# Performance work log

Hardware: AMD Instinct MI355X
Metric: run time of the kernel (lower is better)

Reference implementation:

```python
import jax, jax.numpy as jnp
import numpy as np

N = 50000      # nodes
E = 800000     # directed edges (before self loops)
B = 64         # graphs in batch
F_IN = 128     # input_dim
POS = 16       # pos_dim
H = 4          # heads
C = 64         # hidden_dim (per head)
HC = H * C     # 256
OUT = 128      # output_dim
ENH = F_IN + POS
EPS = 1e-5
NEG_SLOPE = 0.2


def setup_inputs() -> dict:
    key = jax.random.key(0)
    ks = jax.random.split(key, 20)
    s = 0.05
    inp = {
        "x": jax.random.normal(ks[0], (N, F_IN), jnp.float32),
        "edge_index": jax.random.randint(ks[1], (2, E), 0, N, jnp.int32),
        "batch": (jnp.arange(N, dtype=jnp.int32) // ((N + B - 1) // B)).astype(jnp.int32),
        "W_pos": jax.random.normal(ks[2], (2, POS), jnp.float32) * s,
        "b_pos": jnp.zeros((POS,), jnp.float32),
        "W1": jax.random.normal(ks[3], (ENH, HC), jnp.float32) * s,
        "a_src1": jax.random.normal(ks[4], (H, C), jnp.float32) * s,
        "a_dst1": jax.random.normal(ks[5], (H, C), jnp.float32) * s,
        "b1": jnp.zeros((HC,), jnp.float32),
        "gamma1": jnp.ones((HC,), jnp.float32),
        "beta1": jnp.zeros((HC,), jnp.float32),
        "W2": jax.random.normal(ks[6], (HC, HC), jnp.float32) * s,
        "a_src2": jax.random.normal(ks[7], (H, C), jnp.float32) * s,
        "a_dst2": jax.random.normal(ks[8], (H, C), jnp.float32) * s,
        "b2": jnp.zeros((HC,), jnp.float32),
        "gamma2": jnp.ones((HC,), jnp.float32),
        "beta2": jnp.zeros((HC,), jnp.float32),
        "W_fc": jax.random.normal(ks[9], (HC, OUT), jnp.float32) * s,
        "b_fc": jnp.zeros((OUT,), jnp.float32),
    }
    return inp


def _positions(batch):
    # vectorized equivalent of _generate_positions (grid layout per graph)
    ones = jnp.ones((N,), jnp.float32)
    counts = jax.ops.segment_sum(ones, batch, num_segments=B)          # [B]
    starts = jnp.cumsum(counts) - counts                               # [B]
    i = jnp.arange(N, dtype=jnp.float32) - starts[batch]               # index within graph
    gs = jnp.ceil(jnp.sqrt(counts)).astype(jnp.int32)                  # grid size per graph
    g = gs[batch]
    ii = i.astype(jnp.int32)
    row = ii // g
    col = ii % g
    denom = jnp.maximum(g - 1, 1).astype(jnp.float32)
    return jnp.stack([row.astype(jnp.float32) / denom,
                      col.astype(jnp.float32) / denom], axis=1)        # [N, 2]


def _gat(x, W, a_src, a_dst, bias, src, dst):
    # PyG GATConv (concat heads, add_self_loops already in src/dst)
    h = (x @ W).reshape(N, H, C)                                       # [N,H,C]
    alpha_s = jnp.sum(h * a_src, axis=-1)                              # [N,H]
    alpha_d = jnp.sum(h * a_dst, axis=-1)                              # [N,H]
    e = jax.nn.leaky_relu(alpha_s[src] + alpha_d[dst], NEG_SLOPE)      # [Etot,H]
    e_max = jax.ops.segment_max(e, dst, num_segments=N)                # [N,H]
    e_max = jax.lax.stop_gradient(jnp.where(jnp.isfinite(e_max), e_max, 0.0))
    ex = jnp.exp(e - e_max[dst])
    denom = jax.ops.segment_sum(ex, dst, num_segments=N)               # [N,H]
    alpha = ex / denom[dst]                                            # softmax over incoming edges
    msg = h[src] * alpha[:, :, None]                                   # [Etot,H,C]
    out = jax.ops.segment_sum(msg, dst, num_segments=N)                # [N,H,C]
    return out.reshape(N, HC) + bias


def _bn(x, gamma, beta):
    m = jnp.mean(x, axis=0)
    v = jnp.var(x, axis=0)
    return gamma * (x - m) * jax.lax.rsqrt(v + EPS) + beta


def reference(x, edge_index, batch, W_pos, b_pos,
              W1, a_src1, a_dst1, b1, gamma1, beta1,
              W2, a_src2, a_dst2, b2, gamma2, beta2,
              W_fc, b_fc):
    pos = _positions(batch)
    pe = pos @ W_pos + b_pos                                           # [N,POS]
    h = jnp.concatenate([x, pe], axis=1)                               # [N,ENH]
    loops = jnp.arange(N, dtype=edge_index.dtype)
    src = jnp.concatenate([edge_index[0], loops])
    dst = jnp.concatenate([edge_index[1], loops])
    h = jax.nn.elu(_bn(_gat(h, W1, a_src1, a_dst1, b1, src, dst), gamma1, beta1))
    h = jax.nn.elu(_bn(_gat(h, W2, a_src2, a_dst2, b2, src, dst), gamma2, beta2))
    # global mean pool per graph
    counts = jax.ops.segment_sum(jnp.ones((N,), h.dtype), batch, num_segments=B)
    pooled = jax.ops.segment_sum(h, batch, num_segments=B) / counts[:, None]
    return pooled @ W_fc + b_fc                                        # [B,OUT]
```

## Files before the change

kernel.cpp:

```cpp
#include <hip/hip_runtime.h>
#include <math.h>

#define ENH_PAD 160
#define POSD 16
#define DEG_CAP 64
#define NSLICE 8
#define KNODES 8

typedef __attribute__((ext_vector_type(8))) __bf16 bf16x8;
typedef __attribute__((ext_vector_type(4))) float f32x4;

__device__ __forceinline__ unsigned short f2bf(float f){
  unsigned int u = __float_as_uint(f);
  u += 0x7FFF + ((u >> 16) & 1);
  return (unsigned short)(u >> 16);
}
__device__ __forceinline__ float bf2f(unsigned short u){
  return __uint_as_float(((unsigned int)u) << 16);
}

__global__ void k_front(const int* __restrict__ batch, int* __restrict__ starts,
                        const int* __restrict__ src, const int* __restrict__ dst,
                        int* __restrict__ cnt, int* __restrict__ csr_src,
                        float* __restrict__ bnP, float* __restrict__ pooled,
                        int N, int E){
  int i = blockIdx.x * blockDim.x + threadIdx.x;
  if (i < 2 * NSLICE * 512) bnP[i] = 0.f;
  if (i < 64 * 256) pooled[i] = 0.f;
  if (i < N){
    int bi = batch[i];
    int bp = (i == 0) ? -1 : batch[i - 1];
    for (int b = bp + 1; b <= bi; ++b) starts[b] = i;
    if (i == N - 1){
      for (int b = bi + 1; b <= 64; ++b) starts[b] = N;
    }
  }
  if (i < E){
    int d = dst[i];
    int slot = atomicAdd(&cnt[d], 1);
    csr_src[(size_t)d * DEG_CAP + slot] = src[i];
  }
}

__global__ __launch_bounds__(256) void k_prep(
    const float* __restrict__ x, const int* __restrict__ batch,
    const int* __restrict__ starts,
    const float* __restrict__ W_pos, const float* __restrict__ b_pos,
    unsigned short* __restrict__ h0,
    const float* __restrict__ W1, const float* __restrict__ W2,
    unsigned short* __restrict__ W1t, unsigned short* __restrict__ W2t,
    int N, int nb4){
  if ((int)blockIdx.x < nb4){
    int n = blockIdx.x * 4 + (threadIdx.x >> 6);
    if (n >= N) return;
    int t = threadIdx.x & 63;
    unsigned short* hrow = h0 + (size_t)n * ENH_PAD;
    if (t < 32){
      const float4* xs = (const float4*)(x + (size_t)n * 128);
      float4 v = xs[t];
      ushort4 o; o.x = f2bf(v.x); o.y = f2bf(v.y); o.z = f2bf(v.z); o.w = f2bf(v.w);
      ((ushort4*)hrow)[t] = o;
    } else if (t < 48){
      int k = t - 32;
      int b = batch[n];
      int st = starts[b];
      int c = starts[b + 1] - st;
      int g = (int)ceilf(sqrtf((float)c));
      int dd = g - 1; if (dd < 1) dd = 1;
      float idn = 1.0f / (float)dd;
      int i = n - st;
      int row = i / g;
      int col = i - row * g;
      float pe = (float)row * idn * W_pos[k] + (float)col * idn * W_pos[POSD + k] + b_pos[k];
      hrow[128 + k] = f2bf(pe);
    } else {
      hrow[144 + (t - 48)] = 0;
    }
  } else {
    int idx = (blockIdx.x - nb4) * 256 + threadIdx.x;
    const int n1 = 256 * ENH_PAD;
    if (idx < n1){
      int n = idx / ENH_PAD, k = idx - n * ENH_PAD;
      W1t[idx] = f2bf((k < 144) ? W1[(size_t)k * 256 + n] : 0.f);
    } else {
      int j = idx - n1;
      if (j < 256 * 256){
        int n = j >> 8, k = j & 255;
        W2t[j] = f2bf(W2[(size_t)k * 256 + n]);
      }
    }
  }
}

#define LDST 40
__global__ __launch_bounds__(256) void k_mfma_gemm(
    const unsigned short* __restrict__ A, const unsigned short* __restrict__ Bt,
    unsigned short* __restrict__ C,
    const float* __restrict__ a_src, const float* __restrict__ a_dst,
    float* __restrict__ alpS, float* __restrict__ alpD, int M, int Kp){
  __shared__ unsigned short As[128 * LDST];
  __shared__ unsigned short Bs[128 * LDST];
  int t = threadIdx.x;
  int lane = t & 63, wave = t >> 6;
  int wm = (wave >> 1) * 64, wn = (wave & 1) * 64;
  int quad = lane >> 4, l16 = lane & 15;
  int row0 = blockIdx.x * 128;
  int n0 = blockIdx.y * 128;

  f32x4 acc[4][4] = {};

  int eA0 = t, eA1 = t + 256;
  for (int kk = 0; kk < Kp; kk += 32){
    #pragma unroll
    for (int rep = 0; rep < 2; ++rep){
      int e = rep ? eA1 : eA0;
      int r = e >> 2, s = e & 3;
      int grow = row0 + r;
      uint4 va = make_uint4(0, 0, 0, 0);
      if (grow < M) va = *(const uint4*)(A + (size_t)grow * Kp + kk + s * 8);
      *(uint4*)&As[r * LDST + s * 8] = va;
      uint4 vb = *(const uint4*)(Bt + (size_t)(n0 + r) * Kp + kk + s * 8);
      *(uint4*)&Bs[r * LDST + s * 8] = vb;
    }
    __syncthreads();
    bf16x8 af[4], bfr[4];
    #pragma unroll
    for (int i = 0; i < 4; ++i)
      af[i] = *(const bf16x8*)&As[(wm + i * 16 + l16) * LDST + quad * 8];
    #pragma unroll
    for (int j = 0; j < 4; ++j)
      bfr[j] = *(const bf16x8*)&Bs[(wn + j * 16 + l16) * LDST + quad * 8];
    #pragma unroll
    for (int i = 0; i < 4; ++i)
      #pragma unroll
      for (int j = 0; j < 4; ++j)
        acc[i][j] = __builtin_amdgcn_mfma_f32_16x16x32_bf16(af[i], bfr[j], acc[i][j], 0, 0, 0);
    __syncthreads();
  }
  #pragma unroll
  for (int i = 0; i < 4; ++i){
    int rbase = row0 + wm + i * 16 + quad * 4;
    #pragma unroll
    for (int j = 0; j < 4; ++j){
      int col = n0 + wn + j * 16 + l16;
      #pragma unroll
      for (int r = 0; r < 4; ++r){
        int row = rbase + r;
        if (row < M) C[(size_t)row * 256 + col] = f2bf(acc[i][j][r]);
      }
    }
  }
  int hda = (n0 + wn) >> 6;
  float asw[4], adw[4];
  #pragma unroll
  for (int j = 0; j < 4; ++j){
    int c = n0 + wn + j * 16 + l16;
    asw[j] = a_src[c];
    adw[j] = a_dst[c];
  }
  #pragma unroll
  for (int i = 0; i < 4; ++i){
    #pragma unroll
    for (int r = 0; r < 4; ++r){
      int row = row0 + wm + i * 16 + quad * 4 + r;
      float ps = acc[i][0][r] * asw[0] + acc[i][1][r] * asw[1]
               + acc[i][2][r] * asw[2] + acc[i][3][r] * asw[3];
      float pd = acc[i][0][r] * adw[0] + acc[i][1][r] * adw[1]
               + acc[i][2][r] * adw[2] + acc[i][3][r] * adw[3];
      ps += __shfl_xor(ps, 1); ps += __shfl_xor(ps, 2);
      ps += __shfl_xor(ps, 4); ps += __shfl_xor(ps, 8);
      pd += __shfl_xor(pd, 1); pd += __shfl_xor(pd, 2);
      pd += __shfl_xor(pd, 4); pd += __shfl_xor(pd, 8);
      if (l16 == 0 && row < M){
        alpS[row * 4 + hda] = ps;
        alpD[row * 4 + hda] = pd;
      }
    }
  }
}

__global__ __launch_bounds__(256) void k_aggregate(const unsigned short* __restrict__ hlin,
                                                   const float* __restrict__ alpS,
                                                   const float* __restrict__ alpD,
                                                   const int* __restrict__ cnt,
                                                   const int* __restrict__ csr_src,
                                                   const float* __restrict__ bias,
                                                   unsigned short* __restrict__ outb,
                                                   float* __restrict__ bnP, int N){
  __shared__ float rs[4][256];
  __shared__ float rq[4][256];
  int wv = threadIdx.x >> 6;
  int lane = threadIdx.x & 63;
  int hd = lane >> 4;
  int hd2 = lane & 3;
  int eloc = lane >> 2;
  const unsigned short* hbase = hlin + (size_t)lane * 4;
  float4 bv = *(const float4*)(bias + lane * 4);

  float s0 = 0.f, s1 = 0.f, s2 = 0.f, s3 = 0.f;
  float q0 = 0.f, q1 = 0.f, q2 = 0.f, q3 = 0.f;

  int nbase = (blockIdx.x * 4 + wv) * KNODES;
  for (int k = 0; k < KNODES; ++k){
    int n = nbase + k;
    if (n >= N) break;
    int beg = n << 6;
    int deg = cnt[n];
    int total = deg + 1;
    float ad2 = alpD[n * 4 + hd2];
    float lsum = 0.f;
    float a0 = 0.f, a1 = 0.f, a2 = 0.f, a3 = 0.f;

    int full = total & ~15;
    for (int base = 0; base < full; base += 16){
      int e = base + eloc;
      int s = (e < deg) ? csr_src[beg + e] : n;
      float xv = alpS[s * 4 + hd2] + ad2;
      float sc = (xv >= 0.f) ? xv : 0.2f * xv;
      float p = __expf(sc);
      lsum += p;
      uint2 v[16];
      #pragma unroll
      for (int j2 = 0; j2 < 16; ++j2){
        int sj = __shfl(s, j2 << 2);
        v[j2] = *(const uint2*)(hbase + (size_t)sj * 256);
      }
      #pragma unroll
      for (int j2 = 0; j2 < 16; ++j2){
        float pj = __shfl(p, (j2 << 2) | hd);
        a0 += pj * __uint_as_float(v[j2].x << 16);
        a1 += pj * __uint_as_float(v[j2].x & 0xFFFF0000u);
        a2 += pj * __uint_as_float(v[j2].y << 16);
        a3 += pj * __uint_as_float(v[j2].y & 0xFFFF0000u);
      }
    }
    int rem = total - full;
    if (rem){
      int e = full + eloc;
      int s = n;
      float p = 0.f;
      if (eloc < rem){
        if (e < deg) s = csr_src[beg + e];
        float xv = alpS[s * 4 + hd2] + ad2;
        float sc = (xv >= 0.f) ? xv : 0.2f * xv;
        p = __expf(sc);
      }
      lsum += p;
      #pragma unroll
      for (int g = 0; g < 4; ++g){
        if (g * 4 < rem){
          uint2 v[4];
          #pragma unroll
          for (int q = 0; q < 4; ++q){
            int j2 = g * 4 + q;
            int sj = __shfl(s, j2 << 2);
            v[q] = *(const uint2*)(hbase + (size_t)sj * 256);
          }
          #pragma unroll
          for (int q = 0; q < 4; ++q){
            int j2 = g * 4 + q;
            float pj = __shfl(p, (j2 << 2) | hd);
            a0 += pj * __uint_as_float(v[q].x << 16);
            a1 += pj * __uint_as_float(v[q].x & 0xFFFF0000u);
            a2 += pj * __uint_as_float(v[q].y << 16);
            a3 += pj * __uint_as_float(v[q].y & 0xFFFF0000u);
          }
        }
      }
    }
    lsum += __shfl_xor(lsum, 4);
    lsum += __shfl_xor(lsum, 8);
    lsum += __shfl_xor(lsum, 16);
    lsum += __shfl_xor(lsum, 32);
    float lh = __shfl(lsum, hd);
    float inv = 1.0f / lh;
    ushort4 o;
    o.x = f2bf(a0 * inv + bv.x);
    o.y = f2bf(a1 * inv + bv.y);
    o.z = f2bf(a2 * inv + bv.z);
    o.w = f2bf(a3 * inv + bv.w);
    *(ushort4*)(outb + (size_t)n * 256 + lane * 4) = o;
    float f0 = bf2f(o.x), f1 = bf2f(o.y), f2 = bf2f(o.z), f3 = bf2f(o.w);
    s0 += f0; s1 += f1; s2 += f2; s3 += f3;
    q0 += f0 * f0; q1 += f1 * f1; q2 += f2 * f2; q3 += f3 * f3;
  }

  int c0 = lane * 4;
  rs[wv][c0 + 0] = s0; rs[wv][c0 + 1] = s1;
  rs[wv][c0 + 2] = s2; rs[wv][c0 + 3] = s3;
  rq[wv][c0 + 0] = q0; rq[wv][c0 + 1] = q1;
  rq[wv][c0 + 2] = q2; rq[wv][c0 + 3] = q3;
  __syncthreads();
  int t = threadIdx.x;
  float s = rs[0][t] + rs[1][t] + rs[2][t] + rs[3][t];
  float q = rq[0][t] + rq[1][t] + rq[2][t] + rq[3][t];
  float* bp = bnP + (size_t)(blockIdx.x & (NSLICE - 1)) * 512;
  atomicAdd(&bp[t], s);
  atomicAdd(&bp[256 + t], q);
}

__global__ __launch_bounds__(256) void k_bn_elu_bf16(
    const unsigned short* __restrict__ in, const float* __restrict__ bnP,
    const float* __restrict__ gamma, const float* __restrict__ beta,
    unsigned short* __restrict__ outb, int N, float invN){
  __shared__ float scs[256], shs[256];
  int t = threadIdx.x;
  float s = 0.f, q = 0.f;
  #pragma unroll
  for (int j = 0; j < NSLICE; ++j){
    s += bnP[j * 512 + t];
    q += bnP[j * 512 + 256 + t];
  }
  float mean = s * invN;
  float var = q * invN - mean * mean;
  float inv = rsqrtf(var + 1e-5f);
  float g = gamma[t];
  scs[t] = g * inv;
  shs[t] = beta[t] - mean * g * inv;
  __syncthreads();
  int idx8 = blockIdx.x * blockDim.x + t;
  int total8 = N * 32;
  for (; idx8 < total8; idx8 += gridDim.x * blockDim.x){
    int c0 = (idx8 * 8) & 255;
    uint4 raw = *(const uint4*)(in + (size_t)idx8 * 8);
    unsigned int rw[4] = {raw.x, raw.y, raw.z, raw.w};
    uint4 outw;
    unsigned int* ow = (unsigned int*)&outw;
    #pragma unroll
    for (int h = 0; h < 4; ++h){
      unsigned int res = 0;
      #pragma unroll
      for (int k = 0; k < 2; ++k){
        int c = c0 + h * 2 + k;
        unsigned short bits = (unsigned short)((rw[h] >> (16 * k)) & 0xFFFF);
        float y = scs[c] * bf2f(bits) + shs[c];
        y = (y > 0.f) ? y : (__expf(y) - 1.f);
        res |= ((unsigned int)f2bf(y)) << (16 * k);
      }
      ow[h] = res;
    }
    *(uint4*)(outb + (size_t)idx8 * 8) = outw;
  }
}

__global__ __launch_bounds__(256) void k_bn_elu_pool(
    const unsigned short* __restrict__ in, const float* __restrict__ bnP,
    const float* __restrict__ gamma, const float* __restrict__ beta,
    const int* __restrict__ batch,
    float* __restrict__ pooled, int N, float invN){
  int t = threadIdx.x;
  float s = 0.f, q = 0.f;
  #pragma unroll
  for (int j = 0; j < NSLICE; ++j){
    s += bnP[j * 512 + t];
    q += bnP[j * 512 + 256 + t];
  }
  float mean = s * invN;
  float var = q * invN - mean * mean;
  float inv = rsqrtf(var + 1e-5f);
  float g = gamma[t];
  float scl = g * inv;
  float shf = beta[t] - mean * scl;
  int nb = gridDim.x;
  int rows = (N + nb - 1) / nb;
  int r0 = blockIdx.x * rows, r1 = min(r0 + rows, N);
  float acc = 0.f; int cur = -1;
  for (int r = r0; r < r1; ++r){
    float y = scl * bf2f(in[(size_t)r * 256 + t]) + shf;
    y = (y > 0.f) ? y : (__expf(y) - 1.f);
    int b = batch[r];
    if (b != cur){
      if (cur >= 0) atomicAdd(&pooled[cur * 256 + t], acc);
      acc = 0.f; cur = b;
    }
    acc += y;
  }
  if (cur >= 0) atomicAdd(&pooled[cur * 256 + t], acc);
}

__global__ __launch_bounds__(128) void k_final(const float* __restrict__ pooled,
                                               const int* __restrict__ starts,
                                               const float* __restrict__ W_fc,
                                               const float* __restrict__ b_fc,
                                               float* __restrict__ out){
  __shared__ float pm[256];
  int b = blockIdx.x;
  int t = threadIdx.x;
  int c = starts[b + 1] - starts[b];
  float ic = (c > 0) ? 1.0f / (float)c : 0.f;
  pm[t] = pooled[b * 256 + t] * ic;
  pm[t + 128] = pooled[b * 256 + t + 128] * ic;
  __syncthreads();
  float acc = b_fc[t];
  #pragma unroll 4
  for (int cc = 0; cc < 256; ++cc) acc += pm[cc] * W_fc[cc * 128 + t];
  out[b * 128 + t] = acc;
}

extern "C" void kernel_launch(void* const* d_in, const int* in_sizes, int n_in,
                              void* d_out, int out_size, void* d_ws, size_t ws_size,
                              hipStream_t stream){
  const float* x      = (const float*)d_in[0];
  const int*   eidx   = (const int*)  d_in[1];
  const int*   batch  = (const int*)  d_in[2];
  const float* W_pos  = (const float*)d_in[3];
  const float* b_pos  = (const float*)d_in[4];
  const float* W1     = (const float*)d_in[5];
  const float* a_src1 = (const float*)d_in[6];
  const float* a_dst1 = (const float*)d_in[7];
  const float* b1     = (const float*)d_in[8];
  const float* gamma1 = (const float*)d_in[9];
  const float* beta1  = (const float*)d_in[10];
  const float* W2     = (const float*)d_in[11];
  const float* a_src2 = (const float*)d_in[12];
  const float* a_dst2 = (const float*)d_in[13];
  const float* b2     = (const float*)d_in[14];
  const float* gamma2 = (const float*)d_in[15];
  const float* beta2  = (const float*)d_in[16];
  const float* W_fc   = (const float*)d_in[17];
  const float* b_fc   = (const float*)d_in[18];
  float* out = (float*)d_out;

  const int N = in_sizes[0] / 128;
  const int E = in_sizes[1] / 2;
  const int* esrc = eidx;
  const int* edst = eidx + E;

  char* w = (char*)d_ws;
  size_t off = 0;
  auto alloc = [&](size_t bytes) -> void* {
    void* p = w + off;
    off = (off + bytes + 255) & ~(size_t)255;
    return p;
  };
  unsigned short* h0   = (unsigned short*)alloc((size_t)N * 256 * 2);
  unsigned short* X2b  = h0;
  unsigned short* X1b  = (unsigned short*)alloc((size_t)N * 256 * 2);
  unsigned short* A1b  = (unsigned short*)alloc((size_t)N * 256 * 2);
  float* alpS    = (float*)alloc((size_t)N * 4 * 4);
  float* alpD    = (float*)alloc((size_t)N * 4 * 4);
  int*   starts  = (int*)  alloc(65 * 4);
  int*   cnt     = (int*)  alloc((size_t)N * 4);
  int*   csr_src = (int*)  alloc((size_t)N * DEG_CAP * 4);
  float* bnP     = (float*)alloc((size_t)2 * NSLICE * 512 * 4);
  float* pooled  = (float*)alloc(64 * 256 * 4);
  unsigned short* W1t = (unsigned short*)alloc(256 * ENH_PAD * 2);
  unsigned short* W2t = (unsigned short*)alloc(256 * 256 * 2);
  float* bnP1 = bnP, *bnP2 = bnP + NSLICE * 512;

  hipMemsetAsync(cnt, 0, (size_t)N * 4, stream);

  int nb4 = (N + 3) / 4;
  int nbagg = (N + KNODES * 4 - 1) / (KNODES * 4);
  const int packb = (256 * ENH_PAD + 256 * 256 + 255) / 256;

  k_front<<<(E + 255) / 256, 256, 0, stream>>>(batch, starts, esrc, edst, cnt, csr_src,
                                               bnP, pooled, N, E);
  k_prep<<<nb4 + packb, 256, 0, stream>>>(x, batch, starts, W_pos, b_pos, h0,
                                          W1, W2, W1t, W2t, N, nb4);

  dim3 ggrid((N + 127) / 128, 2);
  const float invN = 1.0f / (float)N;

  k_mfma_gemm<<<ggrid, 256, 0, stream>>>(h0, W1t, X1b, a_src1, a_dst1, alpS, alpD, N, ENH_PAD);
  k_aggregate<<<nbagg, 256, 0, stream>>>(X1b, alpS, alpD, cnt, csr_src, b1, A1b, bnP1, N);
  k_bn_elu_bf16<<<512, 256, 0, stream>>>(A1b, bnP1, gamma1, beta1, X2b, N, invN);

  k_mfma_gemm<<<ggrid, 256, 0, stream>>>(X2b, W2t, X1b, a_src2, a_dst2, alpS, alpD, N, 256);
  k_aggregate<<<nbagg, 256, 0, stream>>>(X1b, alpS, alpD, cnt, csr_src, b2, A1b, bnP2, N);
  k_bn_elu_pool<<<512, 256, 0, stream>>>(A1b, bnP2, gamma2, beta2, batch, pooled, N, invN);

  k_final<<<64, 128, 0, stream>>>(pooled, starts, W_fc, b_fc, out);
}
```

Baseline: 428.1 us.

## Fuse CSR build and node prep into one init kernel; retune aggregate granularity

Merges the edge-bucketing front kernel and the feature-prep kernel into a single launch. The per-graph starts array it depended on is replaced by binary searches over the sorted batch array, done in prep and in the final kernel. This removes one launch and the dependency between the two. Separately, KNODES drops from 8 to 2 so the aggregate kernel has more blocks with fewer nodes each, and NSLICE doubles the BN partial-sum slices. The cost is a redundant binary search per node thread and more partial-sum slices to reduce.

```diff
diff --git a/kernel.cpp b/kernel.cpp
--- a/kernel.cpp
+++ b/kernel.cpp
@@ -4,8 +4,8 @@
 #define ENH_PAD 160
 #define POSD 16
 #define DEG_CAP 64
-#define NSLICE 8
-#define KNODES 8
+#define NSLICE 16
+#define KNODES 2
 
 typedef __attribute__((ext_vector_type(8))) __bf16 bf16x8;
 typedef __attribute__((ext_vector_type(4))) float f32x4;
@@ -18,40 +18,38 @@
 __device__ __forceinline__ float bf2f(unsigned short u){
   return __uint_as_float(((unsigned int)u) << 16);
 }
-
-__global__ void k_front(const int* __restrict__ batch, int* __restrict__ starts,
-                        const int* __restrict__ src, const int* __restrict__ dst,
-                        int* __restrict__ cnt, int* __restrict__ csr_src,
-                        float* __restrict__ bnP, float* __restrict__ pooled,
-                        int N, int E){
-  int i = blockIdx.x * blockDim.x + threadIdx.x;
-  if (i < 2 * NSLICE * 512) bnP[i] = 0.f;
-  if (i < 64 * 256) pooled[i] = 0.f;
-  if (i < N){
-    int bi = batch[i];
-    int bp = (i == 0) ? -1 : batch[i - 1];
-    for (int b = bp + 1; b <= bi; ++b) starts[b] = i;
-    if (i == N - 1){
-      for (int b = bi + 1; b <= 64; ++b) starts[b] = N;
-    }
-  }
-  if (i < E){
-    int d = dst[i];
-    int slot = atomicAdd(&cnt[d], 1);
-    csr_src[(size_t)d * DEG_CAP + slot] = src[i];
-  }
-}
-
-__global__ __launch_bounds__(256) void k_prep(
-    const float* __restrict__ x, const int* __restrict__ batch,
-    const int* __restrict__ starts,
+__device__ __forceinline__ int lbound(const int* __restrict__ batch, int N, int b){
+  int lo = 0, hi = N;
+  while (lo < hi){
+    int mid = (lo + hi) >> 1;
+    if (batch[mid] < b) lo = mid + 1; else hi = mid;
+  }
+  return lo;
+}
+
+__global__ __launch_bounds__(256) void k_init(
+    const int* __restrict__ batch,
+    const int* __restrict__ src, const int* __restrict__ dst,
+    int* __restrict__ cnt, int* __restrict__ csr_src,
+    float* __restrict__ bnP, float* __restrict__ pooled,
+    const float* __restrict__ x,
     const float* __restrict__ W_pos, const float* __restrict__ b_pos,
     unsigned short* __restrict__ h0,
     const float* __restrict__ W1, const float* __restrict__ W2,
     unsigned short* __restrict__ W1t, unsigned short* __restrict__ W2t,
-    int N, int nb4){
-  if ((int)blockIdx.x < nb4){
-    int n = blockIdx.x * 4 + (threadIdx.x >> 6);
+    int N, int E, int nfb, int nb4){
+  int bx = blockIdx.x;
+  if (bx < nfb){
+    int i = bx * 256 + threadIdx.x;
+    if (i < 2 * NSLICE * 512) bnP[i] = 0.f;
+    if (i < 64 * 256) pooled[i] = 0.f;
+    if (i < E){
+      int d = dst[i];
+      int slot = atomicAdd(&cnt[d], 1);
+      csr_src[(size_t)d * DEG_CAP + slot] = src[i];
+    }
+  } else if (bx < nfb + nb4){
+    int n = (bx - nfb) * 4 + (threadIdx.x >> 6);
     if (n >= N) return;
     int t = threadIdx.x & 63;
     unsigned short* hrow = h0 + (size_t)n * ENH_PAD;
@@ -63,8 +61,8 @@
     } else if (t < 48){
       int k = t - 32;
       int b = batch[n];
-      int st = starts[b];
-      int c = starts[b + 1] - st;
+      int st = lbound(batch, N, b);
+      int c  = lbound(batch, N, b + 1) - st;
       int g = (int)ceilf(sqrtf((float)c));
       int dd = g - 1; if (dd < 1) dd = 1;
       float idn = 1.0f / (float)dd;
@@ -77,7 +75,7 @@
       hrow[144 + (t - 48)] = 0;
     }
   } else {
-    int idx = (blockIdx.x - nb4) * 256 + threadIdx.x;
+    int idx = (bx - nfb - nb4) * 256 + threadIdx.x;
     const int n1 = 256 * ENH_PAD;
     if (idx < n1){
       int n = idx / ENH_PAD, k = idx - n * ENH_PAD;
@@ -201,6 +199,7 @@
   float q0 = 0.f, q1 = 0.f, q2 = 0.f, q3 = 0.f;
 
   int nbase = (blockIdx.x * 4 + wv) * KNODES;
+  #pragma unroll
   for (int k = 0; k < KNODES; ++k){
     int n = nbase + k;
     if (n >= N) break;
@@ -379,14 +378,14 @@
 }
 
 __global__ __launch_bounds__(128) void k_final(const float* __restrict__ pooled,
-                                               const int* __restrict__ starts,
+                                               const int* __restrict__ batch,
                                                const float* __restrict__ W_fc,
                                                const float* __restrict__ b_fc,
-                                               float* __restrict__ out){
+                                               float* __restrict__ out, int N){
   __shared__ float pm[256];
   int b = blockIdx.x;
   int t = threadIdx.x;
-  int c = starts[b + 1] - starts[b];
+  int c = lbound(batch, N, b + 1) - lbound(batch, N, b);
   float ic = (c > 0) ? 1.0f / (float)c : 0.f;
   pm[t] = pooled[b * 256 + t] * ic;
   pm[t + 128] = pooled[b * 256 + t + 128] * ic;
@@ -439,7 +438,6 @@
   unsigned short* A1b  = (unsigned short*)alloc((size_t)N * 256 * 2);
   float* alpS    = (float*)alloc((size_t)N * 4 * 4);
   float* alpD    = (float*)alloc((size_t)N * 4 * 4);
-  int*   starts  = (int*)  alloc(65 * 4);
   int*   cnt     = (int*)  alloc((size_t)N * 4);
   int*   csr_src = (int*)  alloc((size_t)N * DEG_CAP * 4);
   float* bnP     = (float*)alloc((size_t)2 * NSLICE * 512 * 4);
@@ -450,14 +448,14 @@
 
   hipMemsetAsync(cnt, 0, (size_t)N * 4, stream);
 
-  int nb4 = (N + 3) / 4;
-  int nbagg = (N + KNODES * 4 - 1) / (KNODES * 4);
+  const int nfb = (E + 255) / 256;
+  const int nb4 = (N + 3) / 4;
   const int packb = (256 * ENH_PAD + 256 * 256 + 255) / 256;
-
-  k_front<<<(E + 255) / 256, 256, 0, stream>>>(batch, starts, esrc, edst, cnt, csr_src,
-                                               bnP, pooled, N, E);
-  k_prep<<<nb4 + packb, 256, 0, stream>>>(x, batch, starts, W_pos, b_pos, h0,
-                                          W1, W2, W1t, W2t, N, nb4);
+  const int nbagg = (N + KNODES * 4 - 1) / (KNODES * 4);
+
+  k_init<<<nfb + nb4 + packb, 256, 0, stream>>>(batch, esrc, edst, cnt, csr_src,
+                                                bnP, pooled, x, W_pos, b_pos, h0,
+                                                W1, W2, W1t, W2t, N, E, nfb, nb4);
 
   dim3 ggrid((N + 127) / 128, 2);
   const float invN = 1.0f / (float)N;
@@ -470,5 +468,5 @@
   k_aggregate<<<nbagg, 256, 0, stream>>>(X1b, alpS, alpD, cnt, csr_src, b2, A1b, bnP2, N);
   k_bn_elu_pool<<<512, 256, 0, stream>>>(A1b, bnP2, gamma2, beta2, batch, pooled, N, invN);
 
-  k_final<<<64, 128, 0, stream>>>(pooled, starts, W_fc, b_fc, out);
-}
+  k_final<<<64, 128, 0, stream>>>(pooled, batch, W_fc, b_fc, out, N);
+}
```

Result: slower. 455.9 us (+6.5%).

## Fold positional encoding into GEMM epilogue and merge init kernels

Applied to the files above, without the earlier changes.

Precomputes the product of the positional projection with the matching rows of W1 as three 256-vectors. The first GEMM then runs with K=128 on bf16 x only and adds row/col-scaled terms in its epilogue, which removes the padded 160-wide h0 build. The front and prep kernels are merged into one launch. Aggregation now uses fewer nodes per wave (more blocks), BN partial slices double, and the layer-2 input gets a separate buffer. The epilogue recomputes grid positions per row, which adds some integer and sqrt work per tile.

```diff
diff --git a/kernel.cpp b/kernel.cpp
--- a/kernel.cpp
+++ b/kernel.cpp
@@ -1,11 +1,10 @@
 #include <hip/hip_runtime.h>
 #include <math.h>
 
-#define ENH_PAD 160
 #define POSD 16
 #define DEG_CAP 64
-#define NSLICE 8
-#define KNODES 8
+#define NSLICE 16
+#define KNODES 2
 
 typedef __attribute__((ext_vector_type(8))) __bf16 bf16x8;
 typedef __attribute__((ext_vector_type(4))) float f32x4;
@@ -19,85 +18,77 @@
   return __uint_as_float(((unsigned int)u) << 16);
 }
 
-__global__ void k_front(const int* __restrict__ batch, int* __restrict__ starts,
-                        const int* __restrict__ src, const int* __restrict__ dst,
-                        int* __restrict__ cnt, int* __restrict__ csr_src,
-                        float* __restrict__ bnP, float* __restrict__ pooled,
-                        int N, int E){
-  int i = blockIdx.x * blockDim.x + threadIdx.x;
-  if (i < 2 * NSLICE * 512) bnP[i] = 0.f;
-  if (i < 64 * 256) pooled[i] = 0.f;
-  if (i < N){
-    int bi = batch[i];
-    int bp = (i == 0) ? -1 : batch[i - 1];
-    for (int b = bp + 1; b <= bi; ++b) starts[b] = i;
-    if (i == N - 1){
-      for (int b = bi + 1; b <= 64; ++b) starts[b] = N;
-    }
-  }
-  if (i < E){
-    int d = dst[i];
-    int slot = atomicAdd(&cnt[d], 1);
-    csr_src[(size_t)d * DEG_CAP + slot] = src[i];
-  }
-}
-
-__global__ __launch_bounds__(256) void k_prep(
-    const float* __restrict__ x, const int* __restrict__ batch,
-    const int* __restrict__ starts,
+__global__ __launch_bounds__(256) void k_init(
+    const int* __restrict__ batch, int* __restrict__ starts,
+    const int* __restrict__ src, const int* __restrict__ dst,
+    int* __restrict__ cnt, int* __restrict__ csr_src,
+    float* __restrict__ bnP, float* __restrict__ pooled,
+    const float* __restrict__ x, unsigned short* __restrict__ xb,
     const float* __restrict__ W_pos, const float* __restrict__ b_pos,
-    unsigned short* __restrict__ h0,
     const float* __restrict__ W1, const float* __restrict__ W2,
     unsigned short* __restrict__ W1t, unsigned short* __restrict__ W2t,
-    int N, int nb4){
-  if ((int)blockIdx.x < nb4){
-    int n = blockIdx.x * 4 + (threadIdx.x >> 6);
-    if (n >= N) return;
-    int t = threadIdx.x & 63;
-    unsigned short* hrow = h0 + (size_t)n * ENH_PAD;
-    if (t < 32){
-      const float4* xs = (const float4*)(x + (size_t)n * 128);
-      float4 v = xs[t];
-      ushort4 o; o.x = f2bf(v.x); o.y = f2bf(v.y); o.z = f2bf(v.z); o.w = f2bf(v.w);
-      ((ushort4*)hrow)[t] = o;
-    } else if (t < 48){
-      int k = t - 32;
-      int b = batch[n];
-      int st = starts[b];
-      int c = starts[b + 1] - st;
-      int g = (int)ceilf(sqrtf((float)c));
-      int dd = g - 1; if (dd < 1) dd = 1;
-      float idn = 1.0f / (float)dd;
-      int i = n - st;
-      int row = i / g;
-      int col = i - row * g;
-      float pe = (float)row * idn * W_pos[k] + (float)col * idn * W_pos[POSD + k] + b_pos[k];
-      hrow[128 + k] = f2bf(pe);
-    } else {
-      hrow[144 + (t - 48)] = 0;
-    }
+    float* __restrict__ uvw,
+    int N, int E, int nfb, int nxb){
+  int bx = blockIdx.x;
+  int t = threadIdx.x;
+  if (bx < nfb){
+    int i = bx * 256 + t;
+    if (i < 2 * NSLICE * 512) bnP[i] = 0.f;
+    if (i < 64 * 256) pooled[i] = 0.f;
+    if (i < N){
+      int bi = batch[i];
+      int bp = (i == 0) ? -1 : batch[i - 1];
+      for (int b = bp + 1; b <= bi; ++b) starts[b] = i;
+      if (i == N - 1){
+        for (int b = bi + 1; b <= 64; ++b) starts[b] = N;
+      }
+    }
+    if (i < E){
+      int d = dst[i];
+      int slot = atomicAdd(&cnt[d], 1);
+      csr_src[(size_t)d * DEG_CAP + slot] = src[i];
+    }
+  } else if (bx < nfb + nxb){
+    size_t idx8 = (size_t)(bx - nfb) * 256 + t;
+    if (idx8 * 8 < (size_t)N * 128){
+      const float4* xs = (const float4*)(x + idx8 * 8);
+      float4 v0 = xs[0], v1 = xs[1];
+      ushort4 o0, o1;
+      o0.x = f2bf(v0.x); o0.y = f2bf(v0.y); o0.z = f2bf(v0.z); o0.w = f2bf(v0.w);
+      o1.x = f2bf(v1.x); o1.y = f2bf(v1.y); o1.z = f2bf(v1.z); o1.w = f2bf(v1.w);
+      ushort4* od = (ushort4*)(xb + idx8 * 8);
+      od[0] = o0; od[1] = o1;
+    }
+  } else if (bx < nfb + nxb + 128){
+    int idx = (bx - nfb - nxb) * 256 + t;
+    int n = idx >> 7, k = idx & 127;
+    W1t[idx] = f2bf(W1[(size_t)k * 256 + n]);
+  } else if (bx < nfb + nxb + 128 + 256){
+    int j = (bx - nfb - nxb - 128) * 256 + t;
+    int n = j >> 8, k = j & 255;
+    W2t[j] = f2bf(W2[(size_t)k * 256 + n]);
   } else {
-    int idx = (blockIdx.x - nb4) * 256 + threadIdx.x;
-    const int n1 = 256 * ENH_PAD;
-    if (idx < n1){
-      int n = idx / ENH_PAD, k = idx - n * ENH_PAD;
-      W1t[idx] = f2bf((k < 144) ? W1[(size_t)k * 256 + n] : 0.f);
-    } else {
-      int j = idx - n1;
-      if (j < 256 * 256){
-        int n = j >> 8, k = j & 255;
-        W2t[j] = f2bf(W2[(size_t)k * 256 + n]);
-      }
-    }
+    float u = 0.f, v = 0.f, wv = 0.f;
+    #pragma unroll
+    for (int k = 0; k < POSD; ++k){
+      float wc = W1[(size_t)(128 + k) * 256 + t];
+      u  += W_pos[k] * wc;
+      v  += W_pos[POSD + k] * wc;
+      wv += b_pos[k] * wc;
+    }
+    uvw[t] = u; uvw[256 + t] = v; uvw[512 + t] = wv;
   }
 }
 
 #define LDST 40
+template<int POSC>
 __global__ __launch_bounds__(256) void k_mfma_gemm(
     const unsigned short* __restrict__ A, const unsigned short* __restrict__ Bt,
     unsigned short* __restrict__ C,
     const float* __restrict__ a_src, const float* __restrict__ a_dst,
-    float* __restrict__ alpS, float* __restrict__ alpD, int M, int Kp){
+    float* __restrict__ alpS, float* __restrict__ alpD, int M, int Kp,
+    const float* __restrict__ uvw, const int* __restrict__ batch,
+    const int* __restrict__ starts){
   __shared__ unsigned short As[128 * LDST];
   __shared__ unsigned short Bs[128 * LDST];
   int t = threadIdx.x;
@@ -137,6 +128,38 @@
         acc[i][j] = __builtin_amdgcn_mfma_f32_16x16x32_bf16(af[i], bfr[j], acc[i][j], 0, 0, 0);
     __syncthreads();
   }
+
+  if (POSC){
+    float uu[4], vv[4], ww[4];
+    #pragma unroll
+    for (int j = 0; j < 4; ++j){
+      int col = n0 + wn + j * 16 + l16;
+      uu[j] = uvw[col]; vv[j] = uvw[256 + col]; ww[j] = uvw[512 + col];
+    }
+    #pragma unroll
+    for (int i = 0; i < 4; ++i){
+      #pragma unroll
+      for (int r = 0; r < 4; ++r){
+        int row = row0 + wm + i * 16 + quad * 4 + r;
+        if (row < M){
+          int b = batch[row];
+          int st = starts[b];
+          int cc = starts[b + 1] - st;
+          int g = (int)ceilf(sqrtf((float)cc));
+          int dd = g - 1; if (dd < 1) dd = 1;
+          float idn = 1.0f / (float)dd;
+          int ii = row - st;
+          int irow = ii / g;
+          int icol = ii - irow * g;
+          float rn = (float)irow * idn, cn = (float)icol * idn;
+          #pragma unroll
+          for (int j = 0; j < 4; ++j)
+            acc[i][j][r] += rn * uu[j] + cn * vv[j] + ww[j];
+        }
+      }
+    }
+  }
+
   #pragma unroll
   for (int i = 0; i < 4; ++i){
     int rbase = row0 + wm + i * 16 + quad * 4;
@@ -201,6 +224,7 @@
   float q0 = 0.f, q1 = 0.f, q2 = 0.f, q3 = 0.f;
 
   int nbase = (blockIdx.x * 4 + wv) * KNODES;
+  #pragma unroll
   for (int k = 0; k < KNODES; ++k){
     int n = nbase + k;
     if (n >= N) break;
@@ -433,10 +457,10 @@
     off = (off + bytes + 255) & ~(size_t)255;
     return p;
   };
-  unsigned short* h0   = (unsigned short*)alloc((size_t)N * 256 * 2);
-  unsigned short* X2b  = h0;
+  unsigned short* xb   = (unsigned short*)alloc((size_t)N * 128 * 2);
   unsigned short* X1b  = (unsigned short*)alloc((size_t)N * 256 * 2);
   unsigned short* A1b  = (unsigned short*)alloc((size_t)N * 256 * 2);
+  unsigned short* X2b  = (unsigned short*)alloc((size_t)N * 256 * 2);
   float* alpS    = (float*)alloc((size_t)N * 4 * 4);
   float* alpD    = (float*)alloc((size_t)N * 4 * 4);
   int*   starts  = (int*)  alloc(65 * 4);
@@ -444,29 +468,31 @@
   int*   csr_src = (int*)  alloc((size_t)N * DEG_CAP * 4);
   float* bnP     = (float*)alloc((size_t)2 * NSLICE * 512 * 4);
   float* pooled  = (float*)alloc(64 * 256 * 4);
-  unsigned short* W1t = (unsigned short*)alloc(256 * ENH_PAD * 2);
+  unsigned short* W1t = (unsigned short*)alloc(256 * 128 * 2);
   unsigned short* W2t = (unsigned short*)alloc(256 * 256 * 2);
+  float* uvw = (float*)alloc(3 * 256 * 4);
   float* bnP1 = bnP, *bnP2 = bnP + NSLICE * 512;
 
   hipMemsetAsync(cnt, 0, (size_t)N * 4, stream);
 
-  int nb4 = (N + 3) / 4;
-  int nbagg = (N + KNODES * 4 - 1) / (KNODES * 4);
-  const int packb = (256 * ENH_PAD + 256 * 256 + 255) / 256;
-
-  k_front<<<(E + 255) / 256, 256, 0, stream>>>(batch, starts, esrc, edst, cnt, csr_src,
-                                               bnP, pooled, N, E);
-  k_prep<<<nb4 + packb, 256, 0, stream>>>(x, batch, starts, W_pos, b_pos, h0,
-                                          W1, W2, W1t, W2t, N, nb4);
+  const int nfb = (E + 255) / 256;
+  const int nxb = ((N * 128 / 8) + 255) / 256;
+  const int nbagg = (N + KNODES * 4 - 1) / (KNODES * 4);
+
+  k_init<<<nfb + nxb + 128 + 256 + 1, 256, 0, stream>>>(
+      batch, starts, esrc, edst, cnt, csr_src, bnP, pooled,
+      x, xb, W_pos, b_pos, W1, W2, W1t, W2t, uvw, N, E, nfb, nxb);
 
   dim3 ggrid((N + 127) / 128, 2);
   const float invN = 1.0f / (float)N;
 
-  k_mfma_gemm<<<ggrid, 256, 0, stream>>>(h0, W1t, X1b, a_src1, a_dst1, alpS, alpD, N, ENH_PAD);
+  k_mfma_gemm<1><<<ggrid, 256, 0, stream>>>(xb, W1t, X1b, a_src1, a_dst1,
+                                            alpS, alpD, N, 128, uvw, batch, starts);
   k_aggregate<<<nbagg, 256, 0, stream>>>(X1b, alpS, alpD, cnt, csr_src, b1, A1b, bnP1, N);
   k_bn_elu_bf16<<<512, 256, 0, stream>>>(A1b, bnP1, gamma1, beta1, X2b, N, invN);
 
-  k_mfma_gemm<<<ggrid, 256, 0, stream>>>(X2b, W2t, X1b, a_src2, a_dst2, alpS, alpD, N, 256);
+  k_mfma_gemm<0><<<ggrid, 256, 0, stream>>>(X2b, W2t, X1b, a_src2, a_dst2,
+                                            alpS, alpD, N, 256, nullptr, nullptr, nullptr);
   k_aggregate<<<nbagg, 256, 0, stream>>>(X1b, alpS, alpD, cnt, csr_src, b2, A1b, bnP2, N);
   k_bn_elu_pool<<<512, 256, 0, stream>>>(A1b, bnP2, gamma2, beta2, batch, pooled, N, invN);
 
```

Measured after the change: 429.6 us. No clear change (+0.4%).
